# Performance work log

Measured on AMD Instinct MI355X. Metric: run time of the kernel, lower is better.

Reference implementation:

```python
import jax, jax.numpy as jnp
import numpy as np

BN_EPS = 1e-6


def setup_inputs() -> dict:
    key = jax.random.key(0)
    ks = jax.random.split(key, 6)
    B, N, K, D = 4, 40960, 16, 8
    coords = jax.random.normal(ks[0], (B, N, 3), dtype=jnp.float32)
    features = jax.random.normal(ks[1], (B, D, N, 1), dtype=jnp.float32)
    idx = jax.random.randint(ks[2], (B, N, K), 0, N, dtype=jnp.int32)
    dist = jax.random.uniform(ks[3], (B, N, K), dtype=jnp.float32)
    W = jax.random.normal(ks[4], (D, 10), dtype=jnp.float32) * 0.3
    b = jax.random.normal(ks[5], (D,), dtype=jnp.float32) * 0.1
    gamma = jnp.ones((D,), dtype=jnp.float32)
    beta = jnp.zeros((D,), dtype=jnp.float32)
    return {"coords": coords, "features": features, "idx": idx, "dist": dist,
            "W": W, "b": b, "gamma": gamma, "beta": beta}


def _locse(coords, features, idx, dist, W, b, gamma, beta):
    B, N, K = idx.shape
    D = W.shape[0]
    # gather neighbor coords: [B,N,K,3]
    neighbors = jax.vmap(lambda c, i: c[i])(coords, idx)
    center = jnp.broadcast_to(coords[:, :, None, :], (B, N, K, 3))
    # 10-channel relative-position encoding, channels-last [B,N,K,10]
    concat = jnp.concatenate(
        [center, neighbors, center - neighbors, dist[..., None]], axis=-1)
    # 1x1 conv (10 -> d), output [B,D,N,K]
    h = jnp.einsum('bnkc,dc->bdnk', concat, W) + b[None, :, None, None]
    # BatchNorm2d (training-mode batch stats over B,N,K per channel), eps=1e-6
    mean = jnp.mean(h, axis=(0, 2, 3), keepdims=True)
    var = jnp.var(h, axis=(0, 2, 3), keepdims=True)
    h = (h - mean) * jax.lax.rsqrt(var + BN_EPS)
    h = h * gamma[None, :, None, None] + beta[None, :, None, None]
    h = jax.nn.relu(h)
    # concat with broadcast input features -> [B, 2D, N, K]
    feats = jnp.broadcast_to(features, (B, D, N, K))
    return jnp.concatenate([h, feats], axis=1)


def reference(coords, features, idx, dist, W, b, gamma, beta):
    return _locse(coords, features, idx, dist, W, b, gamma, beta)
```

## Files before the change

### kernel.cpp

```cpp
#include <hip/hip_runtime.h>

constexpr int BB = 4;
constexpr int NN = 40960;
constexpr int KK = 16;
constexpr int DD = 8;
constexpr float BN_EPS = 1e-6f;

constexpr int TOTAL4 = BB * NN * (KK / 4);

constexpr int STATS_BLOCKS  = 512;
constexpr int STATS_THREADS = 640;
constexpr int STATS_NTHREADS = STATS_BLOCKS * STATS_THREADS;
constexpr int STATS_ITEMS    = TOTAL4 / STATS_NTHREADS;
static_assert(STATS_ITEMS * STATS_NTHREADS == TOTAL4, "balanced grid");



__global__ __launch_bounds__(STATS_THREADS, 5) void locse_stats_kernel(
    const float* __restrict__ coords, const int* __restrict__ idx,
    const float* __restrict__ dist, const float* __restrict__ W,
    const float* __restrict__ bias, float* __restrict__ partials)
{
    __shared__ float sA[24];
    __shared__ float sB[24];
    __shared__ float sw9[8];
    __shared__ float sbb[8];
    if (threadIdx.x < 24) {
        const int d = threadIdx.x / 3, j = threadIdx.x % 3;
        sA[threadIdx.x] = W[d * 10 + j] + W[d * 10 + 6 + j];
        sB[threadIdx.x] = W[d * 10 + 3 + j] - W[d * 10 + 6 + j];
    }
    if (threadIdx.x < 8) {
        sw9[threadIdx.x] = W[threadIdx.x * 10 + 9];
        sbb[threadIdx.x] = bias[threadIdx.x];
    }
    __syncthreads();

    float sum[8] = {0.f, 0.f, 0.f, 0.f, 0.f, 0.f, 0.f, 0.f};
    float sq[8]  = {0.f, 0.f, 0.f, 0.f, 0.f, 0.f, 0.f, 0.f};

    const int tau = blockIdx.x * STATS_THREADS + threadIdx.x;
    #pragma unroll
    for (int it = 0; it < STATS_ITEMS; ++it) {
        const int t  = tau + it * STATS_NTHREADS;
        const int k4 = t & 3;
        const int bn = t >> 2;
        const int b  = bn / NN;
        const float* cc = coords + (size_t)bn * 3;
        const float cx = cc[0], cy = cc[1], cz = cc[2];

        float cA[8];
        #pragma unroll
        for (int d = 0; d < 8; ++d)
            cA[d] = fmaf(sA[d * 3 + 2], cz,
                    fmaf(sA[d * 3 + 1], cy,
                    fmaf(sA[d * 3 + 0], cx, sbb[d])));

        const int base = (bn << 4) + (k4 << 2);
        const int4   j4 = *reinterpret_cast<const int4*>(idx + base);
        const float4 d4 = *reinterpret_cast<const float4*>(dist + base);
        const int   js[4] = {j4.x, j4.y, j4.z, j4.w};
        const float ds[4] = {d4.x, d4.y, d4.z, d4.w};

        #pragma unroll
        for (int kk = 0; kk < 4; ++kk) {
            const float* nc = coords + ((size_t)b * NN + js[kk]) * 3;
            const float nx = nc[0], ny = nc[1], nz = nc[2];
            #pragma unroll
            for (int d = 0; d < 8; ++d) {
                float h = fmaf(sw9[d], ds[kk],
                          fmaf(sB[d * 3 + 2], nz,
                          fmaf(sB[d * 3 + 1], ny,
                          fmaf(sB[d * 3 + 0], nx, cA[d]))));
                sum[d] += h;
                sq[d]  += h * h;
            }
        }
    }

    #pragma unroll
    for (int v = 0; v < 8; ++v) {
        float s = sum[v], q = sq[v];
        #pragma unroll
        for (int off = 32; off > 0; off >>= 1) {
            s += __shfl_down(s, off, 64);
            q += __shfl_down(q, off, 64);
        }
        sum[v] = s; sq[v] = q;
    }

    __shared__ float wred[STATS_THREADS / 64][16];
    const int lane = threadIdx.x & 63;
    const int wid  = threadIdx.x >> 6;
    if (lane == 0) {
        #pragma unroll
        for (int v = 0; v < 8; ++v) {
            wred[wid][v]     = sum[v];
            wred[wid][8 + v] = sq[v];
        }
    }
    __syncthreads();
    if (threadIdx.x < 16) {
        float s = 0.f;
        #pragma unroll
        for (int w = 0; w < STATS_THREADS / 64; ++w) s += wred[w][threadIdx.x];
        partials[blockIdx.x * 16 + threadIdx.x] = s;
    }
}

__global__ __launch_bounds__(256) void locse_finalize_kernel(
    const float* __restrict__ partials, const float* __restrict__ W,
    const float* __restrict__ bias, const float* __restrict__ gamma,
    const float* __restrict__ beta, float* __restrict__ wp,
    float* __restrict__ bp)
{
    const int t = threadIdx.x;
    const int c = t & 15;
    float acc = 0.f;
    for (int i = t >> 4; i < STATS_BLOCKS; i += 16) acc += partials[i * 16 + c];

    __shared__ float red[256];
    __shared__ float tot[16];
    __shared__ float scale_s[8];
    red[t] = acc;
    __syncthreads();
    if (t < 16) {
        float s = 0.f;
        #pragma unroll
        for (int i = 0; i < 16; ++i) s += red[i * 16 + t];
        tot[t] = s;
    }
    __syncthreads();
    if (t < 8) {
        const float cnt  = (float)BB * (float)NN * (float)KK;
        const float mean = tot[t] / cnt;
        const float var  = tot[8 + t] / cnt - mean * mean;
        const float sc   = gamma[t] * rsqrtf(var + BN_EPS);
        scale_s[t] = sc;
        bp[t] = fmaf(bias[t] - mean, sc, beta[t]);
    }
    __syncthreads();
    if (t < 80) wp[t] = W[t] * scale_s[t / 10];
}

__global__ __launch_bounds__(256) void locse_out_kernel(
    const float* __restrict__ coords, const float* __restrict__ features,
    const int* __restrict__ idx, const float* __restrict__ dist,
    const float* __restrict__ wp, const float* __restrict__ bp,
    float* __restrict__ out)
{
    __shared__ float sA[24];
    __shared__ float sB[24];
    __shared__ float sw9[8];
    __shared__ float sbb[8];
    if (threadIdx.x < 24) {
        const int d = threadIdx.x / 3, j = threadIdx.x % 3;
        sA[threadIdx.x] = wp[d * 10 + j] + wp[d * 10 + 6 + j];
        sB[threadIdx.x] = wp[d * 10 + 3 + j] - wp[d * 10 + 6 + j];
    }
    if (threadIdx.x < 8) {
        sw9[threadIdx.x] = wp[threadIdx.x * 10 + 9];
        sbb[threadIdx.x] = bp[threadIdx.x];
    }
    __syncthreads();

    const int t = blockIdx.x * blockDim.x + threadIdx.x;
    const int k4 = t & 3;
    const int bn = t >> 2;
    const int b  = bn / NN;
    const int n  = bn - b * NN;
    const float* cc = coords + (size_t)bn * 3;
    const float cx = cc[0], cy = cc[1], cz = cc[2];

    float cA[8];
    #pragma unroll
    for (int d = 0; d < 8; ++d)
        cA[d] = fmaf(sA[d * 3 + 2], cz,
                fmaf(sA[d * 3 + 1], cy,
                fmaf(sA[d * 3 + 0], cx, sbb[d])));

    const int base = (bn << 4) + (k4 << 2);
    const int4   j4 = *reinterpret_cast<const int4*>(idx + base);
    const float4 d4 = *reinterpret_cast<const float4*>(dist + base);
    const int   js[4] = {j4.x, j4.y, j4.z, j4.w};
    const float ds[4] = {d4.x, d4.y, d4.z, d4.w};

    float hv[8][4];
    #pragma unroll
    for (int kk = 0; kk < 4; ++kk) {
        const float* nc = coords + ((size_t)b * NN + js[kk]) * 3;
        const float nx = nc[0], ny = nc[1], nz = nc[2];
        #pragma unroll
        for (int d = 0; d < 8; ++d) {
            const float h = fmaf(sw9[d], ds[kk],
                            fmaf(sB[d * 3 + 2], nz,
                            fmaf(sB[d * 3 + 1], ny,
                            fmaf(sB[d * 3 + 0], nx, cA[d]))));
            hv[d][kk] = fmaxf(h, 0.f);
        }
    }

    const size_t outn = (size_t)b * 16 * NN * KK + (size_t)n * KK + (k4 << 2);
    #pragma unroll
    for (int d = 0; d < 8; ++d) {
        *reinterpret_cast<float4*>(out + outn + (size_t)d * NN * KK) =
            make_float4(hv[d][0], hv[d][1], hv[d][2], hv[d][3]);
    }
    #pragma unroll
    for (int d = 0; d < 8; ++d) {
        const float f = features[((size_t)b * DD + d) * NN + n];
        *reinterpret_cast<float4*>(out + outn + (size_t)(8 + d) * NN * KK) =
            make_float4(f, f, f, f);
    }
}

extern "C" void kernel_launch(void* const* d_in, const int* in_sizes, int n_in,
                              void* d_out, int out_size, void* d_ws, size_t ws_size,
                              hipStream_t stream) {
    const float* coords   = (const float*)d_in[0];
    const float* features = (const float*)d_in[1];
    const int*   idx      = (const int*)d_in[2];
    const float* dist     = (const float*)d_in[3];
    const float* W        = (const float*)d_in[4];
    const float* bias     = (const float*)d_in[5];
    const float* gamma    = (const float*)d_in[6];
    const float* beta     = (const float*)d_in[7];
    float* out = (float*)d_out;

    float* wsf      = (float*)d_ws;
    float* partials = wsf;
    float* wp       = wsf + STATS_BLOCKS * 16;
    float* bp       = wp + 80;

    locse_stats_kernel<<<dim3(STATS_BLOCKS), dim3(STATS_THREADS), 0, stream>>>(
        coords, idx, dist, W, bias, partials);
    locse_finalize_kernel<<<dim3(1), dim3(256), 0, stream>>>(
        partials, W, bias, gamma, beta, wp, bp);

    const int blocks = TOTAL4 / 256;
    locse_out_kernel<<<dim3(blocks), dim3(256), 0, stream>>>(
        coords, features, idx, dist, wp, bp, out);
}
```

Before: 262.7 us.

## Pad coords to float4 and move feature-broadcast writes into the stats pass

Adds a pre-pass that copies coords into a 16-byte-aligned float4 workspace, so the gathers of center and neighbor coordinates become single vector loads instead of three scalar loads. The broadcast-feature half of the output is now written during the stats kernel rather than the output kernel, which spreads the output stores across both passes. The cost is an extra kernel launch and a copy of the coords, and the new path depends on the workspace being large enough, with a fallback to the old path otherwise.

New measurement: 249.1 us (median of 2 runs). 5.2% less time.

```diff
diff --git a/kernel.cpp b/kernel.cpp
--- a/kernel.cpp
+++ b/kernel.cpp
@@ -6,20 +6,41 @@
 constexpr int DD = 8;
 constexpr float BN_EPS = 1e-6f;
 
+constexpr int PTS    = BB * NN;
 constexpr int TOTAL4 = BB * NN * (KK / 4);
 
-constexpr int STATS_BLOCKS  = 512;
-constexpr int STATS_THREADS = 640;
+constexpr int STATS_BLOCKS   = 512;
+constexpr int STATS_THREADS  = 640;
 constexpr int STATS_NTHREADS = STATS_BLOCKS * STATS_THREADS;
 constexpr int STATS_ITEMS    = TOTAL4 / STATS_NTHREADS;
 static_assert(STATS_ITEMS * STATS_NTHREADS == TOTAL4, "balanced grid");
 
-
-
+typedef float f32x4 __attribute__((ext_vector_type(4)));
+
+constexpr int    WS_WP     = STATS_BLOCKS * 16;
+constexpr int    WS_BP     = WS_WP + 80;
+constexpr int    WS_CP     = 8448;
+constexpr size_t WS_NEEDED = (size_t)(WS_CP + 4 * PTS) * sizeof(float);
+
+
+__global__ __launch_bounds__(256) void pad_coords_kernel(
+    const float* __restrict__ coords, float* __restrict__ cp)
+{
+    const int i = blockIdx.x * blockDim.x + threadIdx.x;
+    if (i < PTS) {
+        const float* s = coords + (size_t)i * 3;
+        const f32x4 v = {s[0], s[1], s[2], 0.f};
+        *reinterpret_cast<f32x4*>(cp + (size_t)i * 4) = v;
+    }
+}
+
+template <bool PADDED>
 __global__ __launch_bounds__(STATS_THREADS, 5) void locse_stats_kernel(
-    const float* __restrict__ coords, const int* __restrict__ idx,
+    const float* __restrict__ coords, const float* __restrict__ cp,
+    const float* __restrict__ features, const int* __restrict__ idx,
     const float* __restrict__ dist, const float* __restrict__ W,
-    const float* __restrict__ bias, float* __restrict__ partials)
+    const float* __restrict__ bias, float* __restrict__ partials,
+    float* __restrict__ out)
 {
     __shared__ float sA[24];
     __shared__ float sB[24];
@@ -46,8 +67,16 @@
         const int k4 = t & 3;
         const int bn = t >> 2;
         const int b  = bn / NN;
-        const float* cc = coords + (size_t)bn * 3;
-        const float cx = cc[0], cy = cc[1], cz = cc[2];
+        const int n  = bn - b * NN;
+
+        float cx, cy, cz;
+        if (PADDED) {
+            const f32x4 c4 = *reinterpret_cast<const f32x4*>(cp + (size_t)bn * 4);
+            cx = c4.x; cy = c4.y; cz = c4.z;
+        } else {
+            const float* cc = coords + (size_t)bn * 3;
+            cx = cc[0]; cy = cc[1]; cz = cc[2];
+        }
 
         float cA[8];
         #pragma unroll
@@ -64,8 +93,15 @@
 
         #pragma unroll
         for (int kk = 0; kk < 4; ++kk) {
-            const float* nc = coords + ((size_t)b * NN + js[kk]) * 3;
-            const float nx = nc[0], ny = nc[1], nz = nc[2];
+            float nx, ny, nz;
+            if (PADDED) {
+                const f32x4 nb4 = *reinterpret_cast<const f32x4*>(
+                    cp + ((size_t)b * NN + js[kk]) * 4);
+                nx = nb4.x; ny = nb4.y; nz = nb4.z;
+            } else {
+                const float* nc = coords + ((size_t)b * NN + js[kk]) * 3;
+                nx = nc[0]; ny = nc[1]; nz = nc[2];
+            }
             #pragma unroll
             for (int d = 0; d < 8; ++d) {
                 float h = fmaf(sw9[d], ds[kk],
@@ -75,6 +111,14 @@
                 sum[d] += h;
                 sq[d]  += h * h;
             }
+        }
+
+        const size_t outn = (size_t)b * 16 * NN * KK + (size_t)n * KK + (k4 << 2);
+        #pragma unroll
+        for (int d = 0; d < 8; ++d) {
+            const float f = features[((size_t)b * DD + d) * NN + n];
+            *reinterpret_cast<float4*>(out + outn + (size_t)(8 + d) * NN * KK) =
+                make_float4(f, f, f, f);
         }
     }
 
@@ -143,8 +187,9 @@
     if (t < 80) wp[t] = W[t] * scale_s[t / 10];
 }
 
+template <bool PADDED>
 __global__ __launch_bounds__(256) void locse_out_kernel(
-    const float* __restrict__ coords, const float* __restrict__ features,
+    const float* __restrict__ coords, const float* __restrict__ cp,
     const int* __restrict__ idx, const float* __restrict__ dist,
     const float* __restrict__ wp, const float* __restrict__ bp,
     float* __restrict__ out)
@@ -164,13 +209,20 @@
     }
     __syncthreads();
 
-    const int t = blockIdx.x * blockDim.x + threadIdx.x;
+    const int t  = blockIdx.x * blockDim.x + threadIdx.x;
     const int k4 = t & 3;
     const int bn = t >> 2;
     const int b  = bn / NN;
     const int n  = bn - b * NN;
-    const float* cc = coords + (size_t)bn * 3;
-    const float cx = cc[0], cy = cc[1], cz = cc[2];
+
+    float cx, cy, cz;
+    if (PADDED) {
+        const f32x4 c4 = *reinterpret_cast<const f32x4*>(cp + (size_t)bn * 4);
+        cx = c4.x; cy = c4.y; cz = c4.z;
+    } else {
+        const float* cc = coords + (size_t)bn * 3;
+        cx = cc[0]; cy = cc[1]; cz = cc[2];
+    }
 
     float cA[8];
     #pragma unroll
@@ -188,8 +240,15 @@
     float hv[8][4];
     #pragma unroll
     for (int kk = 0; kk < 4; ++kk) {
-        const float* nc = coords + ((size_t)b * NN + js[kk]) * 3;
-        const float nx = nc[0], ny = nc[1], nz = nc[2];
+        float nx, ny, nz;
+        if (PADDED) {
+            const f32x4 nb4 = *reinterpret_cast<const f32x4*>(
+                cp + ((size_t)b * NN + js[kk]) * 4);
+            nx = nb4.x; ny = nb4.y; nz = nb4.z;
+        } else {
+            const float* nc = coords + ((size_t)b * NN + js[kk]) * 3;
+            nx = nc[0]; ny = nc[1]; nz = nc[2];
+        }
         #pragma unroll
         for (int d = 0; d < 8; ++d) {
             const float h = fmaf(sw9[d], ds[kk],
@@ -205,12 +264,6 @@
     for (int d = 0; d < 8; ++d) {
         *reinterpret_cast<float4*>(out + outn + (size_t)d * NN * KK) =
             make_float4(hv[d][0], hv[d][1], hv[d][2], hv[d][3]);
-    }
-    #pragma unroll
-    for (int d = 0; d < 8; ++d) {
-        const float f = features[((size_t)b * DD + d) * NN + n];
-        *reinterpret_cast<float4*>(out + outn + (size_t)(8 + d) * NN * KK) =
-            make_float4(f, f, f, f);
     }
 }
 
@@ -229,15 +282,30 @@
 
     float* wsf      = (float*)d_ws;
     float* partials = wsf;
-    float* wp       = wsf + STATS_BLOCKS * 16;
-    float* bp       = wp + 80;
-
-    locse_stats_kernel<<<dim3(STATS_BLOCKS), dim3(STATS_THREADS), 0, stream>>>(
-        coords, idx, dist, W, bias, partials);
-    locse_finalize_kernel<<<dim3(1), dim3(256), 0, stream>>>(
-        partials, W, bias, gamma, beta, wp, bp);
-
-    const int blocks = TOTAL4 / 256;
-    locse_out_kernel<<<dim3(blocks), dim3(256), 0, stream>>>(
-        coords, features, idx, dist, wp, bp, out);
-}
+    float* wp       = wsf + WS_WP;
+    float* bp       = wsf + WS_BP;
+    float* cp       = wsf + WS_CP;
+
+    const bool padded = ws_size >= WS_NEEDED;
+    const int out_blocks = TOTAL4 / 256;
+
+    if (padded) {
+        pad_coords_kernel<<<dim3((PTS + 255) / 256), dim3(256), 0, stream>>>(
+            coords, cp);
+        locse_stats_kernel<true>
+            <<<dim3(STATS_BLOCKS), dim3(STATS_THREADS), 0, stream>>>(
+                coords, cp, features, idx, dist, W, bias, partials, out);
+        locse_finalize_kernel<<<dim3(1), dim3(256), 0, stream>>>(
+            partials, W, bias, gamma, beta, wp, bp);
+        locse_out_kernel<true><<<dim3(out_blocks), dim3(256), 0, stream>>>(
+            coords, cp, idx, dist, wp, bp, out);
+    } else {
+        locse_stats_kernel<false>
+            <<<dim3(STATS_BLOCKS), dim3(STATS_THREADS), 0, stream>>>(
+                coords, cp, features, idx, dist, W, bias, partials, out);
+        locse_finalize_kernel<<<dim3(1), dim3(256), 0, stream>>>(
+            partials, W, bias, gamma, beta, wp, bp);
+        locse_out_kernel<false><<<dim3(out_blocks), dim3(256), 0, stream>>>(
+            coords, cp, idx, dist, wp, bp, out);
+    }
+}
```
